# Kernel optimization log

Hardware: AMD Instinct MI355X
Metric: run time of the kernel (lower is better)

## Reference

```python
import jax, jax.numpy as jnp
import numpy as np

MODEL_DIM = 512
NUM_HEADS = 8
HEAD_DIM = 64
INNER = NUM_HEADS * HEAD_DIM  # 512 == MODEL_DIM -> projection is Identity


def setup_inputs() -> dict:
    key = jax.random.key(0)
    ks = jax.random.split(key, 7)
    B, T = 2, 4096
    x = jax.random.normal(ks[0], (B, T, MODEL_DIM), dtype=jnp.float32)
    s = 1.0 / np.sqrt(MODEL_DIM)
    Wq = jax.random.normal(ks[1], (MODEL_DIM, INNER), dtype=jnp.float32) * s
    Wk = jax.random.normal(ks[2], (MODEL_DIM, INNER), dtype=jnp.float32) * s
    Wv = jax.random.normal(ks[3], (MODEL_DIM, INNER), dtype=jnp.float32) * s
    bq = jax.random.normal(ks[4], (INNER,), dtype=jnp.float32) * 0.01
    bk = jax.random.normal(ks[5], (INNER,), dtype=jnp.float32) * 0.01
    bv = jax.random.normal(ks[6], (INNER,), dtype=jnp.float32) * 0.01
    return {"x": x, "Wq": Wq, "bq": bq, "Wk": Wk, "bk": bk, "Wv": Wv, "bv": bv}


def reference(x, Wq, bq, Wk, bk, Wv, bv):
    B, T, _ = x.shape
    # project and split heads: [B, H, T, D]
    q = (x @ Wq + bq).reshape(B, T, NUM_HEADS, HEAD_DIM).transpose(0, 2, 1, 3)
    k = (x @ Wk + bk).reshape(B, T, NUM_HEADS, HEAD_DIM).transpose(0, 2, 1, 3)
    v = (x @ Wv + bv).reshape(B, T, NUM_HEADS, HEAD_DIM).transpose(0, 2, 1, 3)
    scale = 1.0 / np.sqrt(HEAD_DIM).astype(np.float32)
    attn = jnp.einsum('bhqd,bhkd->bhqk', q, k) * scale  # [B,H,Tq,Tkv]
    attn = jax.nn.softmax(attn, axis=-1)
    out = jnp.einsum('bhqk,bhkd->bhqd', attn, v)        # [B,H,Tq,D]
    out = out.transpose(0, 2, 1, 3).reshape(B, T, INNER)
    return out  # projection is Identity since INNER == MODEL_DIM
```

## Files before the change

### kernel.cpp

```cpp
#include <hip/hip_runtime.h>
#include <hip/hip_bf16.h>


typedef __attribute__((ext_vector_type(8)))  _Float16 half8;
typedef __attribute__((ext_vector_type(2)))  __fp16   fp16x2;
typedef __attribute__((ext_vector_type(4)))  float    f32x4;
typedef __attribute__((ext_vector_type(16))) float    f32x16;
typedef __attribute__((ext_vector_type(2)))  int      i32x2;

#define TSEQ 4096
#define DH   64
#define NH   8
#define MD   512

#if __has_builtin(__builtin_amdgcn_exp2f)
__device__ inline float fexp2(float x){ return __builtin_amdgcn_exp2f(x); }
#else
__device__ inline float fexp2(float x){ float r; asm("v_exp_f32 %0, %1\n\ts_nop 1" : "=v"(r) : "v"(x)); return r; }
#endif

union H2U { fp16x2 h; unsigned int u; };
__device__ inline unsigned int pkrtz(float a, float b){
  H2U c; c.h = __builtin_amdgcn_cvt_pkrtz(a, b); return c.u;
}

#if __has_builtin(__builtin_amdgcn_permlane32_swap)
__device__ inline void plswap(unsigned int &a, unsigned int &b){
  i32x2 r = __builtin_amdgcn_permlane32_swap((int)a, (int)b, false, false);
  a = (unsigned int)r[0]; b = (unsigned int)r[1];
}
#else
__device__ inline void plswap(unsigned int &a, unsigned int &b){
  asm volatile("s_nop 1\n\tv_permlane32_swap_b32 %0, %1\n\ts_nop 1" : "+v"(a), "+v"(b));
}
#endif

union U4H8 { uint4 u; half8 h; };

#define AS3U(p) ((__attribute__((address_space(3))) unsigned int*)(p))
#define AS1U(p) ((const __attribute__((address_space(1))) unsigned int*)(p))

__global__ __launch_bounds__(256) void k_prep(const float* __restrict__ x, _Float16* __restrict__ xh,
                                              const float* __restrict__ Wq, const float* __restrict__ Wk,
                                              const float* __restrict__ Wv, _Float16* __restrict__ wt){
  const int bid = blockIdx.x;
  if (bid < 2048){
    int i = (bid*256 + threadIdx.x)*8;
    float4 a = *(const float4*)(x+i);
    float4 b = *(const float4*)(x+i+4);
    half8 o;
    o[0]=(_Float16)a.x; o[1]=(_Float16)a.y; o[2]=(_Float16)a.z; o[3]=(_Float16)a.w;
    o[4]=(_Float16)b.x; o[5]=(_Float16)b.y; o[6]=(_Float16)b.z; o[7]=(_Float16)b.w;
    *(half8*)(xh+i) = o;
    return;
  }
  __shared__ float tile[32][33];
  const int bid2 = bid - 2048;
  const int mat = bid2 >> 8;
  const int rem = bid2 & 255;
  const float* W = mat==0 ? Wq : (mat==1 ? Wk : Wv);
  const int n0 = (rem&15)*32, k0 = (rem>>4)*32;
  const int tx = threadIdx.x & 31, ty = threadIdx.x >> 5;
  #pragma unroll
  for (int i=0;i<4;i++){ int k = ty*4+i; tile[k][tx] = W[(size_t)(k0+k)*MD + n0 + tx]; }
  __syncthreads();
  _Float16* dst = wt + (size_t)mat*MD*MD;
  #pragma unroll
  for (int i=0;i<4;i++){ int n = ty*4+i; dst[(size_t)(n0+n)*MD + k0 + tx] = (_Float16)tile[tx][n]; }
}

__global__ __launch_bounds__(256,2) void k_qkv(const _Float16* __restrict__ xh, const _Float16* __restrict__ wt,
              const float* __restrict__ bq, const float* __restrict__ bk, const float* __restrict__ bv,
              _Float16* __restrict__ qout, _Float16* __restrict__ kout, _Float16* __restrict__ vout){
  __shared__ alignas(16) _Float16 Ash[2][128*64];
  __shared__ alignas(16) _Float16 Bsh[2][128*64];
  const int tid = threadIdx.x, w = tid>>6, l = tid&63;
  const int fr = l&15, hi = l>>4;
  const int nt = blockIdx.x, mt = blockIdx.y;
  const int mat = nt>>2;
  const int n0  = (nt&3)*128;
  const int m0  = mt*128;
  const _Float16* W = wt + (size_t)mat*MD*MD;
  const int wr = (w>>1)*64, wc = (w&1)*64;

  f32x4 acc[4][4];
  #pragma unroll
  for (int a=0;a<4;a++)
    #pragma unroll
    for (int b=0;b<4;b++) acc[a][b] = (f32x4){0.f,0.f,0.f,0.f};

#define QSTAGE(k0_, buf) do { \
    _Pragma("unroll") \
    for (int i_=0;i_<4;i_++){ \
      int slot_ = tid + i_*256; \
      int row_ = slot_>>3, seg_ = (slot_&7) ^ (row_&7); \
      __builtin_amdgcn_global_load_lds(AS1U(xh + (size_t)(m0+row_)*MD + (k0_) + seg_*8), \
          AS3U((char*)&Ash[buf][0] + slot_*16), 16, 0, 0); \
      __builtin_amdgcn_global_load_lds(AS1U(W + (size_t)(n0+row_)*MD + (k0_) + seg_*8), \
          AS3U((char*)&Bsh[buf][0] + slot_*16), 16, 0, 0); \
    } \
  } while(0)

  QSTAGE(0, 0);

  for (int ks0=0; ks0<8; ks0++){
    const int cur = ks0&1;
    __syncthreads();
    if (ks0+1 < 8) QSTAGE((ks0+1)*64, cur^1);
    const _Float16* Ab = &Ash[cur][0];
    const _Float16* Bb = &Bsh[cur][0];
    #pragma unroll
    for (int ks=0;ks<2;ks++){
      half8 af[4], bfr[4];
      #pragma unroll
      for (int mi=0;mi<4;mi++){
        int row = wr + mi*16 + fr;
        af[mi] = *(const half8*)&Ab[row*64 + (((ks*4+hi) ^ (row&7))<<3)];
      }
      #pragma unroll
      for (int ni=0;ni<4;ni++){
        int row = wc + ni*16 + fr;
        bfr[ni] = *(const half8*)&Bb[row*64 + (((ks*4+hi) ^ (row&7))<<3)];
      }
      #pragma unroll
      for (int mi=0;mi<4;mi++)
        #pragma unroll
        for (int ni=0;ni<4;ni++)
          acc[mi][ni] = __builtin_amdgcn_mfma_f32_16x16x32_f16(af[mi], bfr[ni], acc[mi][ni], 0,0,0);
    }
  }
#undef QSTAGE

  const float* bias = mat==0 ? bq : (mat==1 ? bk : bv);
  if (mat==1){
    #pragma unroll
    for (int ni=0;ni<4;ni++){
      int n_in = n0 + wc + ni*16 + fr;
      float bb = bias[n_in];
      int h = n_in>>6, d = n_in&63;
      #pragma unroll
      for (int mi=0;mi<4;mi++)
        #pragma unroll
        for (int r=0;r<4;r++){
          int m = m0 + wr + mi*16 + hi*4 + r;
          float v = acc[mi][ni][r] + bb;
          int b_ = m>>12, t = m&4095;
          kout[ ((((size_t)(b_*NH + h))*8 + (d>>3))*TSEQ + t)*8 + (d&7) ] = (_Float16)v;
        }
    }
  } else if (mat==2){
    #pragma unroll
    for (int ni=0;ni<4;ni++){
      int n_in = n0 + wc + ni*16 + fr;
      float bb = bias[n_in];
      int h = n_in>>6, d = n_in&63;
      #pragma unroll
      for (int mi=0;mi<4;mi++)
        #pragma unroll
        for (int r=0;r<4;r++){
          int m = m0 + wr + mi*16 + hi*4 + r;
          float v = (acc[mi][ni][r] + bb)*0.0625f;
          int b_ = m>>12, t = m&4095;
          vout[ ((((size_t)(b_*NH + h))*512 + (t>>3))*64 + d)*8 + (t&7) ] = (_Float16)v;
        }
    }
  } else {
    const float scl = 0.125f*1.4426950408889634f;
    #pragma unroll
    for (int ni=0;ni<4;ni++){
      int n_in = n0 + wc + ni*16 + fr;
      float bb = bias[n_in];
      int h = n_in>>6, d = n_in&63;
      #pragma unroll
      for (int mi=0;mi<4;mi++)
        #pragma unroll
        for (int r=0;r<4;r++){
          int m = m0 + wr + mi*16 + hi*4 + r;
          float v = (acc[mi][ni][r] + bb)*scl;
          int b_ = m>>12, t = m&4095;
          qout[ ((size_t)((b_*NH + h)*TSEQ + t))*DH + d ] = (_Float16)v;
        }
    }
  }
}

__global__ __launch_bounds__(256,2) void k_attn(const _Float16* __restrict__ qb_, const _Float16* __restrict__ ktg,
                                                const _Float16* __restrict__ vtg, float* __restrict__ out){
  __shared__ alignas(16) _Float16 Ksh[2*8192];
  __shared__ alignas(16) _Float16 Vsh[2*8192];
  const int tid = threadIdx.x, w = tid>>6, l = tid&63;
  const int ln31 = l&31, lh = l>>5;

  const int bid = blockIdx.x;
  const int swz = ((bid&7)<<6) | (bid>>3);
  const int bh = swz>>5, qblk = swz&31;

  const _Float16* Q  = qb_ + (size_t)bh*TSEQ*DH;
  const _Float16* Kt = ktg + (size_t)bh*8*TSEQ*8;
  const _Float16* Vt = vtg + (size_t)bh*512*64*8;
  const int q0 = qblk*128 + w*32;

  half8 qf[4];
  #pragma unroll
  for (int ds=0;ds<4;ds++)
    qf[ds] = *(const half8*)(Q + (size_t)(q0 + ln31)*DH + ds*16 + lh*8);

  f32x16 of0, of1;
  #pragma unroll
  for (int r=0;r<16;r++){ of0[r]=0.f; of1[r]=0.f; }
  const f32x16 fzero = of0;
  float psum = 0.f;

  const int NT = TSEQ/128;
  const int kbase = lh*1024 + ln31*8;
  const int vbase = lh*512  + ln31*8;

#define STAGE(kt, buf) do { \
    const int k0_ = (kt)*128; \
    _Pragma("unroll") \
    for (int i_=0;i_<4;i_++){ \
      int base_ = i_*256 + w*64; \
      int slot_ = base_ + l; \
      int krow_ = slot_&127, kseg_ = slot_>>7; \
      __builtin_amdgcn_global_load_lds(AS1U(Kt + ((size_t)kseg_*TSEQ + k0_ + krow_)*8), \
          AS3U((char*)Ksh + (buf)*16384 + base_*16), 16, 0, 0); \
      __builtin_amdgcn_global_load_lds(AS1U(Vt + ((size_t)slot_ + k0_*8)*8), \
          AS3U((char*)Vsh + (buf)*16384 + base_*16), 16, 0, 0); \
    } \
  } while(0)

  STAGE(0, 0);

  for (int kt=0; kt<NT; kt++){
    const int cur = kt&1;
    __syncthreads();
    if (kt+1 < NT) STAGE(kt+1, cur^1);

    const _Float16* Kb = &Ksh[cur*8192];
    const _Float16* Vb = &Vsh[cur*8192];

    #pragma unroll
    for (int pair=0; pair<2; pair++){
      half8 kf[8], vf[8];
      #pragma unroll
      for (int ds=0;ds<4;ds++){
        kf[ds]   = *(const half8*)&Kb[kbase + ds*2048 + (pair*2+0)*256];
        kf[4+ds] = *(const half8*)&Kb[kbase + ds*2048 + (pair*2+1)*256];
      }
      #pragma unroll
      for (int ea=0;ea<4;ea++){
        vf[2*ea]   = *(const half8*)&Vb[vbase + (pair*4+ea)*1024];
        vf[2*ea+1] = *(const half8*)&Vb[vbase + (pair*4+ea)*1024 + 256];
      }

      f32x16 s0 = __builtin_amdgcn_mfma_f32_32x32x16_f16(kf[0], qf[0], fzero, 0,0,0);
      f32x16 s1 = __builtin_amdgcn_mfma_f32_32x32x16_f16(kf[4], qf[0], fzero, 0,0,0);
      #pragma unroll
      for (int ds=1;ds<4;ds++){
        s0 = __builtin_amdgcn_mfma_f32_32x32x16_f16(kf[ds],   qf[ds], s0, 0,0,0);
        s1 = __builtin_amdgcn_mfma_f32_32x32x16_f16(kf[4+ds], qf[ds], s1, 0,0,0);
      }

      unsigned int wv[16];
      #pragma unroll
      for (int m=0;m<2;m++){
        #pragma unroll
        for (int c=0;c<4;c++){
          float v0_ = m ? s1[4*c+0] : s0[4*c+0];
          float v1_ = m ? s1[4*c+1] : s0[4*c+1];
          float v2_ = m ? s1[4*c+2] : s0[4*c+2];
          float v3_ = m ? s1[4*c+3] : s0[4*c+3];
          float e0 = fexp2(v0_);
          float e1 = fexp2(v1_);
          float e2 = fexp2(v2_);
          float e3 = fexp2(v3_);
          psum += (e0+e1)+(e2+e3);
          wv[m*8+2*c+0] = pkrtz(e0, e1);
          wv[m*8+2*c+1] = pkrtz(e2, e3);
        }
      }

      #pragma unroll
      for (int m=0;m<2;m++){
        #pragma unroll
        for (int e=0;e<2;e++){
          unsigned int a0 = wv[m*8+4*e+0], a1 = wv[m*8+4*e+1];
          unsigned int b0 = wv[m*8+4*e+2], b1 = wv[m*8+4*e+3];
          plswap(a0, b0);
          plswap(a1, b1);
          U4H8 pf; pf.u.x=a0; pf.u.y=a1; pf.u.z=b0; pf.u.w=b1;
          const int sl = m*2 + e;
          of0 = __builtin_amdgcn_mfma_f32_32x32x16_f16(vf[2*sl],   pf.h, of0, 0,0,0);
          of1 = __builtin_amdgcn_mfma_f32_32x32x16_f16(vf[2*sl+1], pf.h, of1, 0,0,0);
        }
      }
    }
  }

  psum += __shfl_xor(psum, 32);
  float inv = 16.0f / psum;

  const int b_ = bh>>3, h = bh&7;
  float* o = out + ((size_t)(b_*TSEQ + q0 + ln31))*MD + h*DH;
  #pragma unroll
  for (int rr=0;rr<4;rr++){
    float4 o4 = { of0[4*rr+0]*inv, of0[4*rr+1]*inv, of0[4*rr+2]*inv, of0[4*rr+3]*inv };
    *(float4*)(o + rr*8 + lh*4) = o4;
  }
  #pragma unroll
  for (int rr=0;rr<4;rr++){
    float4 o4 = { of1[4*rr+0]*inv, of1[4*rr+1]*inv, of1[4*rr+2]*inv, of1[4*rr+3]*inv };
    *(float4*)(o + 32 + rr*8 + lh*4) = o4;
  }
#undef STAGE
}

extern "C" void kernel_launch(void* const* d_in, const int* in_sizes, int n_in,
                              void* d_out, int out_size, void* d_ws, size_t ws_size,
                              hipStream_t stream) {
  const float* x  = (const float*)d_in[0];
  const float* Wq = (const float*)d_in[1];
  const float* bq = (const float*)d_in[2];
  const float* Wk = (const float*)d_in[3];
  const float* bk = (const float*)d_in[4];
  const float* Wv = (const float*)d_in[5];
  const float* bv = (const float*)d_in[6];
  float* out = (float*)d_out;

  char* ws = (char*)d_ws;
  _Float16* xh = (_Float16*)(ws);
  _Float16* wt = (_Float16*)(ws + ((size_t)8<<20));
  _Float16* qb = (_Float16*)(ws + ((size_t)10<<20));
  _Float16* kb = (_Float16*)(ws + ((size_t)18<<20));
  _Float16* vtg= (_Float16*)(ws + ((size_t)26<<20));

  k_prep<<<2816, 256, 0, stream>>>(x, xh, Wq, Wk, Wv, wt);
  k_qkv<<<dim3(12,64), 256, 0, stream>>>(xh, wt, bq, bk, bv, qb, kb, vtg);
  k_attn<<<512, 256, 0, stream>>>(qb, kb, vtg, out);
}
```

Measured before the change: 114.6 us.

## Enlarge attention blocks, single-buffer QKV GEMM, sum softmax via fp16 dot

The attention kernel now runs 512-thread blocks that each cover 256 queries, so the K/V tiles in shared memory are shared by eight waves instead of four, and staging needs half as many loads per thread. The QKV GEMM drops its shared-memory double buffer and raises occupancy to three blocks per CU, so global loads no longer overlap with MFMA work inside a block. The softmax row sum is now taken from the packed fp16 probabilities with a dot2 against ones, split over two accumulators. This makes the normaliser match the rounded values fed to the PV matmul and drops some FP32 adds. The risk is that the GEMM's added synchronisation exposes load latency, and the larger attention blocks add barrier cost.

```diff
diff --git a/kernel.cpp b/kernel.cpp
--- a/kernel.cpp
+++ b/kernel.cpp
@@ -22,6 +22,16 @@
 union H2U { fp16x2 h; unsigned int u; };
 __device__ inline unsigned int pkrtz(float a, float b){
   H2U c; c.h = __builtin_amdgcn_cvt_pkrtz(a, b); return c.u;
+}
+
+__device__ inline float fdot2w(unsigned int u, float acc){
+#if __has_builtin(__builtin_amdgcn_fdot2)
+  H2U a, b; a.u = u; b.u = 0x3C003C00u;
+  return __builtin_amdgcn_fdot2(a.h, b.h, acc, false);
+#else
+  H2U a; a.u = u;
+  return acc + (float)a.h[0] + (float)a.h[1];
+#endif
 }
 
 #if __has_builtin(__builtin_amdgcn_permlane32_swap)
@@ -69,11 +79,11 @@
   for (int i=0;i<4;i++){ int n = ty*4+i; dst[(size_t)(n0+n)*MD + k0 + tx] = (_Float16)tile[tx][n]; }
 }
 
-__global__ __launch_bounds__(256,2) void k_qkv(const _Float16* __restrict__ xh, const _Float16* __restrict__ wt,
+__global__ __launch_bounds__(256,3) void k_qkv(const _Float16* __restrict__ xh, const _Float16* __restrict__ wt,
               const float* __restrict__ bq, const float* __restrict__ bk, const float* __restrict__ bv,
               _Float16* __restrict__ qout, _Float16* __restrict__ kout, _Float16* __restrict__ vout){
-  __shared__ alignas(16) _Float16 Ash[2][128*64];
-  __shared__ alignas(16) _Float16 Bsh[2][128*64];
+  __shared__ alignas(16) _Float16 Ash[128*64];
+  __shared__ alignas(16) _Float16 Bsh[128*64];
   const int tid = threadIdx.x, w = tid>>6, l = tid&63;
   const int fr = l&15, hi = l>>4;
   const int nt = blockIdx.x, mt = blockIdx.y;
@@ -89,38 +99,34 @@
     #pragma unroll
     for (int b=0;b<4;b++) acc[a][b] = (f32x4){0.f,0.f,0.f,0.f};
 
-#define QSTAGE(k0_, buf) do { \
+#define QSTAGE(k0_) do { \
     _Pragma("unroll") \
     for (int i_=0;i_<4;i_++){ \
       int slot_ = tid + i_*256; \
       int row_ = slot_>>3, seg_ = (slot_&7) ^ (row_&7); \
       __builtin_amdgcn_global_load_lds(AS1U(xh + (size_t)(m0+row_)*MD + (k0_) + seg_*8), \
-          AS3U((char*)&Ash[buf][0] + slot_*16), 16, 0, 0); \
+          AS3U((char*)&Ash[0] + slot_*16), 16, 0, 0); \
       __builtin_amdgcn_global_load_lds(AS1U(W + (size_t)(n0+row_)*MD + (k0_) + seg_*8), \
-          AS3U((char*)&Bsh[buf][0] + slot_*16), 16, 0, 0); \
+          AS3U((char*)&Bsh[0] + slot_*16), 16, 0, 0); \
     } \
   } while(0)
 
-  QSTAGE(0, 0);
-
   for (int ks0=0; ks0<8; ks0++){
-    const int cur = ks0&1;
     __syncthreads();
-    if (ks0+1 < 8) QSTAGE((ks0+1)*64, cur^1);
-    const _Float16* Ab = &Ash[cur][0];
-    const _Float16* Bb = &Bsh[cur][0];
+    QSTAGE(ks0*64);
+    __syncthreads();
     #pragma unroll
     for (int ks=0;ks<2;ks++){
       half8 af[4], bfr[4];
       #pragma unroll
       for (int mi=0;mi<4;mi++){
         int row = wr + mi*16 + fr;
-        af[mi] = *(const half8*)&Ab[row*64 + (((ks*4+hi) ^ (row&7))<<3)];
+        af[mi] = *(const half8*)&Ash[row*64 + (((ks*4+hi) ^ (row&7))<<3)];
       }
       #pragma unroll
       for (int ni=0;ni<4;ni++){
         int row = wc + ni*16 + fr;
-        bfr[ni] = *(const half8*)&Bb[row*64 + (((ks*4+hi) ^ (row&7))<<3)];
+        bfr[ni] = *(const half8*)&Bsh[row*64 + (((ks*4+hi) ^ (row&7))<<3)];
       }
       #pragma unroll
       for (int mi=0;mi<4;mi++)
@@ -184,7 +190,7 @@
   }
 }
 
-__global__ __launch_bounds__(256,2) void k_attn(const _Float16* __restrict__ qb_, const _Float16* __restrict__ ktg,
+__global__ __launch_bounds__(512,2) void k_attn(const _Float16* __restrict__ qb_, const _Float16* __restrict__ ktg,
                                                 const _Float16* __restrict__ vtg, float* __restrict__ out){
   __shared__ alignas(16) _Float16 Ksh[2*8192];
   __shared__ alignas(16) _Float16 Vsh[2*8192];
@@ -192,13 +198,13 @@
   const int ln31 = l&31, lh = l>>5;
 
   const int bid = blockIdx.x;
-  const int swz = ((bid&7)<<6) | (bid>>3);
-  const int bh = swz>>5, qblk = swz&31;
+  const int swz = ((bid&7)<<5) | (bid>>3);
+  const int bh = swz>>4, qblk = swz&15;
 
   const _Float16* Q  = qb_ + (size_t)bh*TSEQ*DH;
   const _Float16* Kt = ktg + (size_t)bh*8*TSEQ*8;
   const _Float16* Vt = vtg + (size_t)bh*512*64*8;
-  const int q0 = qblk*128 + w*32;
+  const int q0 = qblk*256 + w*32;
 
   half8 qf[4];
   #pragma unroll
@@ -209,7 +215,7 @@
   #pragma unroll
   for (int r=0;r<16;r++){ of0[r]=0.f; of1[r]=0.f; }
   const f32x16 fzero = of0;
-  float psum = 0.f;
+  float psum0 = 0.f, psum1 = 0.f;
 
   const int NT = TSEQ/128;
   const int kbase = lh*1024 + ln31*8;
@@ -218,8 +224,8 @@
 #define STAGE(kt, buf) do { \
     const int k0_ = (kt)*128; \
     _Pragma("unroll") \
-    for (int i_=0;i_<4;i_++){ \
-      int base_ = i_*256 + w*64; \
+    for (int i_=0;i_<2;i_++){ \
+      int base_ = i_*512 + w*64; \
       int slot_ = base_ + l; \
       int krow_ = slot_&127, kseg_ = slot_>>7; \
       __builtin_amdgcn_global_load_lds(AS1U(Kt + ((size_t)kseg_*TSEQ + k0_ + krow_)*8), \
@@ -274,9 +280,12 @@
           float e1 = fexp2(v1_);
           float e2 = fexp2(v2_);
           float e3 = fexp2(v3_);
-          psum += (e0+e1)+(e2+e3);
-          wv[m*8+2*c+0] = pkrtz(e0, e1);
-          wv[m*8+2*c+1] = pkrtz(e2, e3);
+          unsigned int u0 = pkrtz(e0, e1);
+          unsigned int u1 = pkrtz(e2, e3);
+          wv[m*8+2*c+0] = u0;
+          wv[m*8+2*c+1] = u1;
+          if (m==0){ psum0 = fdot2w(u0, psum0); psum0 = fdot2w(u1, psum0); }
+          else     { psum1 = fdot2w(u0, psum1); psum1 = fdot2w(u1, psum1); }
         }
       }
 
@@ -297,6 +306,7 @@
     }
   }
 
+  float psum = psum0 + psum1;
   psum += __shfl_xor(psum, 32);
   float inv = 16.0f / psum;
 
@@ -336,5 +346,5 @@
 
   k_prep<<<2816, 256, 0, stream>>>(x, xh, Wq, Wk, Wv, wt);
   k_qkv<<<dim3(12,64), 256, 0, stream>>>(xh, wt, bq, bk, bv, qb, kb, vtg);
-  k_attn<<<512, 256, 0, stream>>>(qb, kb, vtg, out);
-}
+  k_attn<<<256, 512, 0, stream>>>(qb, kb, vtg, out);
+}
```

After: 118.6 us. 1.03x slower.
